# Kernel tuning notes

Measured on AMD Instinct MI355X. Metric: run time of the kernel, lower is better.

Reference implementation:

```python
import jax, jax.numpy as jnp
import numpy as np

# GCN over dependency trees (aryehgigi/gcn-over-pruned-trees), eval mode:
# dropout = identity, rnn=False, dep_dim=0, no_adj=False.
# Per layer l: Ax = adj @ x ; AxW = Linear_l(Ax) + Linear_l(x) (bias counted twice,
# faithful to `self.W[l](Ax) + self.W[l](gcn_inputs)`) ; AxW /= (adj.sum(2)+1) ; relu.

B, L = 128, 256
VOCAB, EMB, POSV, POSD, NERV, NERD, MEM = 50000, 300, 52, 30, 20, 30, 200
IN_DIM = EMB + POSD + NERD  # 360


def setup_inputs() -> dict:
    key = jax.random.key(0)
    ks = jax.random.split(key, 11)
    words = jax.random.randint(ks[0], (B, L), 0, VOCAB)
    pos = jax.random.randint(ks[1], (B, L), 0, POSV)
    ner = jax.random.randint(ks[2], (B, L), 0, NERV)
    adj = (jax.random.uniform(ks[3], (B, L, L)) < 0.05).astype(jnp.float32)
    emb_W = jax.random.normal(ks[4], (VOCAB, EMB), jnp.float32) * 0.1
    pos_W = jax.random.normal(ks[5], (POSV, POSD), jnp.float32) * 0.1
    ner_W = jax.random.normal(ks[6], (NERV, NERD), jnp.float32) * 0.1
    W0 = jax.random.normal(ks[7], (MEM, IN_DIM), jnp.float32) * (1.0 / np.sqrt(IN_DIM))
    b0 = jnp.zeros((MEM,), jnp.float32)
    W1 = jax.random.normal(ks[8], (MEM, MEM), jnp.float32) * (1.0 / np.sqrt(MEM))
    b1 = jnp.zeros((MEM,), jnp.float32)
    return {"words": words, "pos": pos, "ner": ner, "adj": adj,
            "emb_W": emb_W, "pos_W": pos_W, "ner_W": ner_W,
            "W0": W0, "b0": b0, "W1": W1, "b1": b1}


def reference(words, pos, ner, adj, emb_W, pos_W, ner_W, W0, b0, W1, b1):
    # embedding lookups + concat -> [B, L, IN_DIM]
    x = jnp.concatenate([emb_W[words], pos_W[pos], ner_W[ner]], axis=2)
    denom = jnp.sum(adj, axis=2, keepdims=True) + 1.0  # [B, L, 1]
    mask = ((jnp.sum(adj, axis=2) + jnp.sum(adj, axis=1)) == 0)[..., None]  # [B, L, 1]
    for W, b in ((W0, b0), (W1, b1)):
        Ax = jnp.einsum('bij,bjd->bid', adj, x)  # message passing
        # W(Ax) + W(x) == (Ax + x) @ W.T + 2*b  (bias applied twice, as in source)
        h = (jnp.einsum('bld,md->blm', Ax + x, W) + 2.0 * b) / denom
        x = jax.nn.relu(h)
    return (x, mask)
```

## Files before the change

kernel.cpp:

```cpp
#include <hip/hip_runtime.h>
#include <hip/hip_bf16.h>
#include <stdint.h>

typedef __attribute__((ext_vector_type(8))) short short8;
typedef __attribute__((ext_vector_type(4))) float f32x4;

#define NB 128
#define NL 256
#define NROWS 32768
#define IN_DIM 360
#define KP1 384
#define MEM 200
#define NP 256
#define OUT_X (NROWS * MEM)
#define YTP 264
#define BUFSZ 20480
#define YTOFF 40960
#define RSOFF 74752


__device__ __forceinline__ unsigned short f2b(float f) {
    unsigned u = __builtin_bit_cast(unsigned, f);
    unsigned r = (u + 0x7FFFu + ((u >> 16) & 1u)) >> 16;
    return (unsigned short)r;
}

__device__ __forceinline__ void gl16(const void* g, void* l) {
    __builtin_amdgcn_global_load_lds((const __attribute__((address_space(1))) unsigned*)g,
                                     (__attribute__((address_space(3))) unsigned*)l, 16, 0, 0);
}

__device__ __forceinline__ short8 gather_chunk(int chunk, const float* __restrict__ er,
                                               const float* __restrict__ pr,
                                               const float* __restrict__ nr) {
    float v[8];
    if (chunk < 37) {
        const float* s = er + chunk * 8;
        float4 a = *(const float4*)s;
        float4 b = *(const float4*)(s + 4);
        v[0] = a.x; v[1] = a.y; v[2] = a.z; v[3] = a.w;
        v[4] = b.x; v[5] = b.y; v[6] = b.z; v[7] = b.w;
    } else if (chunk == 37) {
        float4 a = *(const float4*)(er + 296);
        v[0] = a.x; v[1] = a.y; v[2] = a.z; v[3] = a.w;
        v[4] = 0.f; v[5] = 0.f; v[6] = 0.f; v[7] = 0.f;
    } else if (chunk <= 41) {
        int k0 = chunk * 8 - 304;
        #pragma unroll
        for (int i = 0; i < 8; ++i) v[i] = (k0 + i < 30) ? pr[k0 + i] : 0.f;
    } else if (chunk <= 45) {
        int k0 = chunk * 8 - 336;
        #pragma unroll
        for (int i = 0; i < 8; ++i) v[i] = (k0 + i < 30) ? nr[k0 + i] : 0.f;
    } else {
        #pragma unroll
        for (int i = 0; i < 8; ++i) v[i] = 0.f;
    }
    short8 r;
    #pragma unroll
    for (int i = 0; i < 8; ++i) r[i] = (short)f2b(v[i]);
    return r;
}

__global__ void prep_weights(const float* __restrict__ W0, const float* __restrict__ W1,
                             short* __restrict__ W0p, short* __restrict__ W1p) {
    int idx = blockIdx.x * 256 + threadIdx.x;
    if (idx < NP * KP1) {
        int n = idx / KP1, kp = idx - n * KP1;
        float v = 0.f;
        if (n < MEM) {
            if (kp < 300)                   v = W0[n * IN_DIM + kp];
            else if (kp >= 304 && kp < 334) v = W0[n * IN_DIM + 300 + (kp - 304)];
            else if (kp >= 336 && kp < 366) v = W0[n * IN_DIM + 330 + (kp - 336)];
        }
        W0p[idx] = (short)f2b(v);
    } else {
        int i2 = idx - NP * KP1;
        if (i2 < NP * NP) {
            int n = i2 >> 8, k = i2 & 255;
            float v = (n < MEM && k < MEM) ? W1[n * MEM + k] : 0.f;
            W1p[i2] = (short)f2b(v);
        }
    }
}

__global__ __launch_bounds__(512, 4) void fused0_kernel(
    const short* __restrict__ Bp,
    unsigned short* __restrict__ Sbf,
    const float* __restrict__ bias,
    const int* __restrict__ words, const int* __restrict__ pos, const int* __restrict__ ner,
    const float* __restrict__ embW, const float* __restrict__ posW,
    const float* __restrict__ nerW,
    const float* __restrict__ adj,
    float* __restrict__ maskout, float* __restrict__ dinvg,
    short* __restrict__ x1b) {
    extern __shared__ char smem[];
    unsigned short* Yt = (unsigned short*)(smem + YTOFF);
    float* dinvL = (float*)(smem + RSOFF);
    unsigned* colnzL = (unsigned*)(smem + RSOFF + 1024);

    int bi = blockIdx.x;
    int batch = bi & 127, sl = bi >> 7;
    int tid = threadIdx.x;
    int lane = tid & 63, wid = tid >> 6;
    int wr = wid >> 1, wc = wid & 1;
    int lr = lane & 15, lc = lane >> 4;

    if (tid < 256) dinvL[tid] = 0.f;
    if (tid < 8) colnzL[tid] = 0u;
    __syncthreads();
    {
        const float* adjb = adj + (size_t)batch * NL * NL;
        unsigned short* Sw = Sbf + (size_t)batch * NL * NL;
        #pragma unroll 4
        for (int j = 0; j < 16; ++j) {
            int cidx = j * 512 + tid;
            int r = cidx >> 5, c0 = (cidx & 31) << 3;
            const float* src = adjb + (size_t)r * NL + c0;
            float4 a = *(const float4*)src;
            float4 b = *(const float4*)(src + 4);
            float s8 = a.x + a.y + a.z + a.w + b.x + b.y + b.z + b.w;
            unsigned bits = 0;
            bits |= (a.x != 0.f) ? 1u : 0u;   bits |= (a.y != 0.f) ? 2u : 0u;
            bits |= (a.z != 0.f) ? 4u : 0u;   bits |= (a.w != 0.f) ? 8u : 0u;
            bits |= (b.x != 0.f) ? 16u : 0u;  bits |= (b.y != 0.f) ? 32u : 0u;
            bits |= (b.z != 0.f) ? 64u : 0u;  bits |= (b.w != 0.f) ? 128u : 0u;
            #pragma unroll
            for (int o = 16; o >= 1; o >>= 1) s8 += __shfl_xor(s8, o);
            if ((lane & 31) == 0) atomicAdd(&dinvL[r], s8);
            if (bits) atomicOr(&colnzL[c0 >> 5], bits << (c0 & 31));
            float d0 = a.x + ((c0 + 0 == r) ? 1.f : 0.f);
            float d1 = a.y + ((c0 + 1 == r) ? 1.f : 0.f);
            float d2 = a.z + ((c0 + 2 == r) ? 1.f : 0.f);
            float d3 = a.w + ((c0 + 3 == r) ? 1.f : 0.f);
            float d4 = b.x + ((c0 + 4 == r) ? 1.f : 0.f);
            float d5 = b.y + ((c0 + 5 == r) ? 1.f : 0.f);
            float d6 = b.z + ((c0 + 6 == r) ? 1.f : 0.f);
            float d7 = b.w + ((c0 + 7 == r) ? 1.f : 0.f);
            short8 st;
            st[0] = (short)f2b(d0); st[1] = (short)f2b(d1);
            st[2] = (short)f2b(d2); st[3] = (short)f2b(d3);
            st[4] = (short)f2b(d4); st[5] = (short)f2b(d5);
            st[6] = (short)f2b(d6); st[7] = (short)f2b(d7);
            *(short8*)(Sw + (size_t)r * NL + c0) = st;
        }
    }
    __syncthreads();
    if (tid < 256) {
        float s = dinvL[tid];
        float di = 1.0f / (s + 1.0f);
        dinvL[tid] = di;
        if (sl == 0) {
            unsigned bit = (colnzL[tid >> 5] >> (tid & 31)) & 1u;
            maskout[batch * NL + tid] = (s == 0.f && bit == 0u) ? 1.0f : 0.0f;
            dinvg[batch * NL + tid] = di;
        }
    }

    const short* Bb = Bp + (size_t)sl * 64 * KP1;
    const short* Sb = (const short*)(Sbf + (size_t)batch * NL * NL);

    int r0s = tid >> 2, c0s = tid & 3;
    int r1s = r0s + 128;
    int offA0 = r0s * 64 + (c0s ^ ((r0s >> 1) & 3)) * 16;
    int offA1 = r1s * 64 + (c0s ^ ((r1s >> 1) & 3)) * 16;
    const short* Sp0 = Sb + (size_t)r0s * NL + c0s * 8;
    const short* Sp1 = Sb + (size_t)r1s * NL + c0s * 8;
    int offB = 0; const short* Bpp = nullptr;
    if (tid < 256) {
        int br = tid >> 2, bc = tid & 3;
        offB = 16384 + br * 64 + (bc ^ ((br >> 1) & 3)) * 16;
        Bpp = Bb + (size_t)br * KP1 + bc * 8;
    }

    const float *er0, *pr0, *nr0, *er1, *pr1, *nr1;
    {
        int g0 = batch * NL + r0s, g1 = g0 + 128;
        er0 = embW + (size_t)words[g0] * 300;
        pr0 = posW + (size_t)pos[g0] * 30;
        nr0 = nerW + (size_t)ner[g0] * 30;
        er1 = embW + (size_t)words[g1] * 300;
        pr1 = posW + (size_t)pos[g1] * 30;
        nr1 = nerW + (size_t)ner[g1] * 30;
    }
    #define LOADA(kt, o0, o1) do {                                  \
        int ch_ = (kt) * 4 + c0s;                                   \
        (o0) = gather_chunk(ch_, er0, pr0, nr0);                    \
        (o1) = gather_chunk(ch_, er1, pr1, nr1);                    \
    } while (0)

    f32x4 acc[4][2] = {};
    short8 aR0, aR1, bR;
    LOADA(0, aR0, aR1);
    if (tid < 256) bR = *(const short8*)Bpp;
    *(short8*)(smem + offA0) = aR0;
    *(short8*)(smem + offA1) = aR1;
    if (tid < 256) *(short8*)(smem + offB) = bR;
    LOADA(1, aR0, aR1);
    if (tid < 256) bR = *(const short8*)(Bpp + 32);
    __syncthreads();

    short8 sA0, sA1, sB0, sB1;
    const int nkt = KP1 / 32;
    for (int kt = 0; kt < nkt; ++kt) {
        char* base_ = smem + (kt & 1) * BUFSZ;
        short8 af[4], bf[2];
        #pragma unroll
        for (int mi = 0; mi < 4; ++mi) {
            int row = wr * 64 + mi * 16 + lr;
            int cs = lc ^ ((row >> 1) & 3);
            af[mi] = *(const short8*)(base_ + row * 64 + cs * 16);
        }
        #pragma unroll
        for (int ni = 0; ni < 2; ++ni) {
            int row = wc * 32 + ni * 16 + lr;
            int cs = lc ^ ((row >> 1) & 3);
            bf[ni] = *(const short8*)(base_ + 16384 + row * 64 + cs * 16);
        }
        if (kt + 1 < nkt) {
            char* nb_ = smem + ((kt + 1) & 1) * BUFSZ;
            *(short8*)(nb_ + offA0) = aR0;
            *(short8*)(nb_ + offA1) = aR1;
            if (tid < 256) *(short8*)(nb_ + offB) = bR;
        }
        if (kt + 2 < nkt) {
            LOADA(kt + 2, aR0, aR1);
            if (tid < 256) bR = *(const short8*)(Bpp + (kt + 2) * 32);
        } else if (kt + 2 == nkt) {
            sA0 = *(const short8*)Sp0;
            sA1 = *(const short8*)Sp1;
        } else if (kt + 2 == nkt + 1) {
            sB0 = *(const short8*)(Sp0 + 32);
            sB1 = *(const short8*)(Sp1 + 32);
        }
        #pragma unroll
        for (int mi = 0; mi < 4; ++mi)
            #pragma unroll
            for (int ni = 0; ni < 2; ++ni)
                acc[mi][ni] = __builtin_amdgcn_mfma_f32_16x16x32_bf16(af[mi], bf[ni], acc[mi][ni], 0, 0, 0);
        __syncthreads();
    }
    #undef LOADA

    #pragma unroll
    for (int mi = 0; mi < 4; ++mi)
        #pragma unroll
        for (int ni = 0; ni < 2; ++ni) {
            f32x4 v = acc[mi][ni];
            ushort4 st; st.x = f2b(v[0]); st.y = f2b(v[1]); st.z = f2b(v[2]); st.w = f2b(v[3]);
            int col = wc * 32 + ni * 16 + lr;
            int row0 = wr * 64 + mi * 16 + lc * 4;
            *(ushort4*)(Yt + (size_t)col * YTP + row0) = st;
        }
    *(short8*)(smem + offA0) = sA0;
    *(short8*)(smem + offA1) = sA1;
    sA0 = *(const short8*)(Sp0 + 64);
    sA1 = *(const short8*)(Sp1 + 64);
    __syncthreads();

    f32x4 acc2[4][2] = {};
    #pragma unroll
    for (int kt = 0; kt < 8; ++kt) {
        char* base_ = smem + (kt & 1) * BUFSZ;
        short8 ay[4], bs[2];
        #pragma unroll
        for (int mi = 0; mi < 4; ++mi)
            ay[mi] = *(const short8*)(Yt + (size_t)(mi * 16 + lr) * YTP + kt * 32 + lc * 8);
        #pragma unroll
        for (int ni = 0; ni < 2; ++ni) {
            int row = wid * 32 + ni * 16 + lr;
            int cs = lc ^ ((row >> 1) & 3);
            bs[ni] = *(const short8*)(base_ + row * 64 + cs * 16);
        }
        if (kt + 1 < 8) {
            char* nb_ = smem + ((kt + 1) & 1) * BUFSZ;
            if ((kt & 1) == 0) {
                *(short8*)(nb_ + offA0) = sB0;
                *(short8*)(nb_ + offA1) = sB1;
                if (kt + 3 < 8) {
                    sB0 = *(const short8*)(Sp0 + (kt + 3) * 32);
                    sB1 = *(const short8*)(Sp1 + (kt + 3) * 32);
                }
            } else {
                *(short8*)(nb_ + offA0) = sA0;
                *(short8*)(nb_ + offA1) = sA1;
                if (kt + 3 < 8) {
                    sA0 = *(const short8*)(Sp0 + (kt + 3) * 32);
                    sA1 = *(const short8*)(Sp1 + (kt + 3) * 32);
                }
            }
        }
        #pragma unroll
        for (int mi = 0; mi < 4; ++mi)
            #pragma unroll
            for (int ni = 0; ni < 2; ++ni)
                acc2[mi][ni] = __builtin_amdgcn_mfma_f32_16x16x32_bf16(ay[mi], bs[ni], acc2[mi][ni], 0, 0, 0);
        if (kt + 1 < 8) __syncthreads();
    }

    #pragma unroll
    for (int ni = 0; ni < 2; ++ni) {
        int rloc = wid * 32 + ni * 16 + lr;
        int g = batch * NL + rloc;
        float di = dinvL[rloc];
        #pragma unroll
        for (int mi = 0; mi < 4; ++mi) {
            int col0 = sl * 64 + mi * 16 + lc * 4;
            float4 bv;
            if (col0 < MEM) bv = *(const float4*)(bias + col0);
            else { bv.x = 0.f; bv.y = 0.f; bv.z = 0.f; bv.w = 0.f; }
            f32x4 z = acc2[mi][ni];
            ushort4 st;
            st.x = f2b(fmaxf((z[0] + 2.f * bv.x) * di, 0.f));
            st.y = f2b(fmaxf((z[1] + 2.f * bv.y) * di, 0.f));
            st.z = f2b(fmaxf((z[2] + 2.f * bv.z) * di, 0.f));
            st.w = f2b(fmaxf((z[3] + 2.f * bv.w) * di, 0.f));
            *(ushort4*)((unsigned short*)x1b + (size_t)g * NP + col0) = st;
        }
    }
}

__global__ __launch_bounds__(512, 4) void fused1_kernel(
    const short* __restrict__ A,
    const short* __restrict__ Bp,
    const unsigned short* __restrict__ Sbf,
    const float* __restrict__ dinv, const float* __restrict__ bias,
    float* __restrict__ outx) {
    extern __shared__ char smem[];
    unsigned short* Yt = (unsigned short*)(smem + YTOFF);

    int bi = blockIdx.x;
    int batch = bi & 127, sl = bi >> 7;
    int tid = threadIdx.x;
    int lane = tid & 63, wid = tid >> 6;
    int wr = wid >> 1, wc = wid & 1;
    int lr = lane & 15, lc = lane >> 4;

    const short* Ab = A + (size_t)batch * NL * NP;
    const short* Bb = Bp + (size_t)sl * 64 * NP;
    const short* Sb = (const short*)(Sbf + (size_t)batch * NL * NL);

    int li0 = tid, li1 = tid + 512;
    int rA0 = li0 >> 2, cA0 = (li0 & 3) ^ ((rA0 >> 1) & 3);
    int rA1 = li1 >> 2, cA1 = (li1 & 3) ^ ((rA1 >> 1) & 3);
    const short* srcA0 = Ab + (size_t)rA0 * NP + cA0 * 8;
    const short* srcA1 = Ab + (size_t)rA1 * NP + cA1 * 8;
    const short* srcS0 = Sb + (size_t)rA0 * NL + cA0 * 8;
    const short* srcS1 = Sb + (size_t)rA1 * NL + cA1 * 8;
    const short* srcB = nullptr;
    if (wid < 4) {
        int rB = tid >> 2, cB = (tid & 3) ^ ((rB >> 1) & 3);
        srcB = Bb + (size_t)rB * NP + cB * 8;
    }
    int dA0 = (wid * 64) * 16;
    int dA1 = (512 + wid * 64) * 16;
    int dB  = 16384 + (wid * 64) * 16;

    #define STAGE1(b, kt) do {                                       \
        char* bb_ = smem + (b) * BUFSZ;                              \
        gl16(srcA0 + (kt) * 32, bb_ + dA0);                          \
        gl16(srcA1 + (kt) * 32, bb_ + dA1);                          \
        if (wid < 4) gl16(srcB + (kt) * 32, bb_ + dB);               \
    } while (0)
    #define STAGES(b, kt) do {                                       \
        char* bb_ = smem + (b) * BUFSZ;                              \
        gl16(srcS0 + (kt) * 32, bb_ + dA0);                          \
        gl16(srcS1 + (kt) * 32, bb_ + dA1);                          \
    } while (0)
    #define WAITBAR() do {                                           \
        asm volatile("s_waitcnt vmcnt(0)" ::: "memory");             \
        __builtin_amdgcn_sched_barrier(0);                           \
        __builtin_amdgcn_s_barrier();                                \
    } while (0)

    f32x4 acc[4][2] = {};
    STAGE1(0, 0);
    WAITBAR();
    #pragma unroll
    for (int kt = 0; kt < 8; ++kt) {
        if (kt + 1 < 8) STAGE1((kt + 1) & 1, kt + 1);
        char* base_ = smem + (kt & 1) * BUFSZ;
        short8 af[4], bf[2];
        #pragma unroll
        for (int mi = 0; mi < 4; ++mi) {
            int row = wr * 64 + mi * 16 + lr;
            int cs = lc ^ ((row >> 1) & 3);
            af[mi] = *(const short8*)(base_ + row * 64 + cs * 16);
        }
        #pragma unroll
        for (int ni = 0; ni < 2; ++ni) {
            int row = wc * 32 + ni * 16 + lr;
            int cs = lc ^ ((row >> 1) & 3);
            bf[ni] = *(const short8*)(base_ + 16384 + row * 64 + cs * 16);
        }
        #pragma unroll
        for (int mi = 0; mi < 4; ++mi)
            #pragma unroll
            for (int ni = 0; ni < 2; ++ni)
                acc[mi][ni] = __builtin_amdgcn_mfma_f32_16x16x32_bf16(af[mi], bf[ni], acc[mi][ni], 0, 0, 0);
        WAITBAR();
    }

    STAGES(0, 0);
    #pragma unroll
    for (int mi = 0; mi < 4; ++mi)
        #pragma unroll
        for (int ni = 0; ni < 2; ++ni) {
            f32x4 v = acc[mi][ni];
            ushort4 st; st.x = f2b(v[0]); st.y = f2b(v[1]); st.z = f2b(v[2]); st.w = f2b(v[3]);
            int col = wc * 32 + ni * 16 + lr;
            int row0 = wr * 64 + mi * 16 + lc * 4;
            *(ushort4*)(Yt + (size_t)col * YTP + row0) = st;
        }
    asm volatile("s_waitcnt vmcnt(0)" ::: "memory");
    __builtin_amdgcn_sched_barrier(0);
    __syncthreads();

    f32x4 acc2[4][2] = {};
    #pragma unroll
    for (int kt = 0; kt < 8; ++kt) {
        if (kt + 1 < 8) STAGES((kt + 1) & 1, kt + 1);
        char* base_ = smem + (kt & 1) * BUFSZ;
        short8 ay[4], bs[2];
        #pragma unroll
        for (int mi = 0; mi < 4; ++mi)
            ay[mi] = *(const short8*)(Yt + (size_t)(mi * 16 + lr) * YTP + kt * 32 + lc * 8);
        #pragma unroll
        for (int ni = 0; ni < 2; ++ni) {
            int row = wid * 32 + ni * 16 + lr;
            int cs = lc ^ ((row >> 1) & 3);
            bs[ni] = *(const short8*)(base_ + row * 64 + cs * 16);
        }
        #pragma unroll
        for (int mi = 0; mi < 4; ++mi)
            #pragma unroll
            for (int ni = 0; ni < 2; ++ni)
                acc2[mi][ni] = __builtin_amdgcn_mfma_f32_16x16x32_bf16(ay[mi], bs[ni], acc2[mi][ni], 0, 0, 0);
        if (kt + 1 < 8) WAITBAR();
    }
    #undef STAGE1
    #undef STAGES
    #undef WAITBAR

    #pragma unroll
    for (int ni = 0; ni < 2; ++ni) {
        int g = batch * NL + wid * 32 + ni * 16 + lr;
        float di = dinv[g];
        #pragma unroll
        for (int mi = 0; mi < 4; ++mi) {
            int col0 = sl * 64 + mi * 16 + lc * 4;
            if (col0 < MEM) {
                float4 bv = *(const float4*)(bias + col0);
                f32x4 z = acc2[mi][ni];
                float4 o;
                o.x = fmaxf((z[0] + 2.f * bv.x) * di, 0.f);
                o.y = fmaxf((z[1] + 2.f * bv.y) * di, 0.f);
                o.z = fmaxf((z[2] + 2.f * bv.z) * di, 0.f);
                o.w = fmaxf((z[3] + 2.f * bv.w) * di, 0.f);
                *(float4*)(outx + (size_t)g * MEM + col0) = o;
            }
        }
    }
}

extern "C" void kernel_launch(void* const* d_in, const int* in_sizes, int n_in,
                              void* d_out, int out_size, void* d_ws, size_t ws_size,
                              hipStream_t stream) {
    const int*   words = (const int*)d_in[0];
    const int*   pos   = (const int*)d_in[1];
    const int*   ner   = (const int*)d_in[2];
    const float* adj   = (const float*)d_in[3];
    const float* embW  = (const float*)d_in[4];
    const float* posW  = (const float*)d_in[5];
    const float* nerW  = (const float*)d_in[6];
    const float* W0    = (const float*)d_in[7];
    const float* b0    = (const float*)d_in[8];
    const float* W1    = (const float*)d_in[9];
    const float* b1    = (const float*)d_in[10];
    float* out = (float*)d_out;

    char* ws = (char*)d_ws;
    size_t off = 0;
    short* W0p = (short*)(ws + off);        off += (size_t)NP * KP1 * 2;
    short* W1p = (short*)(ws + off);        off += (size_t)NP * NP * 2;
    short* X1b = (short*)(ws + off);        off += (size_t)NROWS * NP * 2;
    float* dinv = (float*)(ws + off);       off += (size_t)NROWS * 4;
    unsigned short* Sbf = (unsigned short*)(ws + off); off += (size_t)NROWS * NL * 2;

    prep_weights<<<(NP * KP1 + NP * NP + 255) / 256, 256, 0, stream>>>(W0, W1, W0p, W1p);

    const int ldsB0 = RSOFF + 1024 + 32;
    const int ldsB1 = YTOFF + 64 * YTP * 2;
    fused0_kernel<<<NB * 4, 512, ldsB0, stream>>>(W0p, Sbf, b0,
                                                  words, pos, ner, embW, posW, nerW,
                                                  adj, out + OUT_X, dinv, X1b);
    fused1_kernel<<<NB * 4, 512, ldsB1, stream>>>(X1b, W1p, Sbf, dinv, b1, out);
}
```

Before: 67.55 us.

## Fuse fp32 adjacency conversion into layer-0 stream, computing row sums inline

Removes the separate prologue that converted the whole fp32 adjacency tile to bf16 (with atomics and two barriers) before the GEMMs. Each thread now loads its own fp32 adjacency chunks just in time inside the pipelined loops, converts them (adding the identity), accumulates row sums and column-nonzero bits, and writes the bf16 copy to global only from the first column slice. Row-degree reciprocals are reduced with shuffles after the second GEMM. The aim is to overlap adjacency conversion with MFMA work and avoid redundant writes, at the cost of more fp32 global reads and more register pressure.

```diff
diff --git a/kernel.cpp b/kernel.cpp
--- a/kernel.cpp
+++ b/kernel.cpp
@@ -28,6 +28,26 @@
 __device__ __forceinline__ void gl16(const void* g, void* l) {
     __builtin_amdgcn_global_load_lds((const __attribute__((address_space(1))) unsigned*)g,
                                      (__attribute__((address_space(3))) unsigned*)l, 16, 0, 0);
+}
+
+__device__ __forceinline__ short8 convS(float4 a, float4 b, int row, int j0, float& rs,
+                                        unsigned* colnzL, bool dobits) {
+    float v[8];
+    v[0] = a.x; v[1] = a.y; v[2] = a.z; v[3] = a.w;
+    v[4] = b.x; v[5] = b.y; v[6] = b.z; v[7] = b.w;
+    rs += v[0] + v[1] + v[2] + v[3] + v[4] + v[5] + v[6] + v[7];
+    if (dobits) {
+        unsigned bits = 0;
+        #pragma unroll
+        for (int i = 0; i < 8; ++i) bits |= (v[i] != 0.f) ? (1u << i) : 0u;
+        if (bits) atomicOr(&colnzL[j0 >> 5], bits << (j0 & 31));
+    }
+    int d = row - j0;
+    if (d >= 0 && d < 8) v[d] += 1.f;
+    short8 st;
+    #pragma unroll
+    for (int i = 0; i < 8; ++i) st[i] = (short)f2b(v[i]);
+    return st;
 }
 
 __device__ __forceinline__ short8 gather_chunk(int chunk, const float* __restrict__ er,
@@ -105,67 +125,20 @@
     int lane = tid & 63, wid = tid >> 6;
     int wr = wid >> 1, wc = wid & 1;
     int lr = lane & 15, lc = lane >> 4;
-
-    if (tid < 256) dinvL[tid] = 0.f;
+    bool s0 = (sl == 0);
+
     if (tid < 8) colnzL[tid] = 0u;
-    __syncthreads();
-    {
-        const float* adjb = adj + (size_t)batch * NL * NL;
-        unsigned short* Sw = Sbf + (size_t)batch * NL * NL;
-        #pragma unroll 4
-        for (int j = 0; j < 16; ++j) {
-            int cidx = j * 512 + tid;
-            int r = cidx >> 5, c0 = (cidx & 31) << 3;
-            const float* src = adjb + (size_t)r * NL + c0;
-            float4 a = *(const float4*)src;
-            float4 b = *(const float4*)(src + 4);
-            float s8 = a.x + a.y + a.z + a.w + b.x + b.y + b.z + b.w;
-            unsigned bits = 0;
-            bits |= (a.x != 0.f) ? 1u : 0u;   bits |= (a.y != 0.f) ? 2u : 0u;
-            bits |= (a.z != 0.f) ? 4u : 0u;   bits |= (a.w != 0.f) ? 8u : 0u;
-            bits |= (b.x != 0.f) ? 16u : 0u;  bits |= (b.y != 0.f) ? 32u : 0u;
-            bits |= (b.z != 0.f) ? 64u : 0u;  bits |= (b.w != 0.f) ? 128u : 0u;
-            #pragma unroll
-            for (int o = 16; o >= 1; o >>= 1) s8 += __shfl_xor(s8, o);
-            if ((lane & 31) == 0) atomicAdd(&dinvL[r], s8);
-            if (bits) atomicOr(&colnzL[c0 >> 5], bits << (c0 & 31));
-            float d0 = a.x + ((c0 + 0 == r) ? 1.f : 0.f);
-            float d1 = a.y + ((c0 + 1 == r) ? 1.f : 0.f);
-            float d2 = a.z + ((c0 + 2 == r) ? 1.f : 0.f);
-            float d3 = a.w + ((c0 + 3 == r) ? 1.f : 0.f);
-            float d4 = b.x + ((c0 + 4 == r) ? 1.f : 0.f);
-            float d5 = b.y + ((c0 + 5 == r) ? 1.f : 0.f);
-            float d6 = b.z + ((c0 + 6 == r) ? 1.f : 0.f);
-            float d7 = b.w + ((c0 + 7 == r) ? 1.f : 0.f);
-            short8 st;
-            st[0] = (short)f2b(d0); st[1] = (short)f2b(d1);
-            st[2] = (short)f2b(d2); st[3] = (short)f2b(d3);
-            st[4] = (short)f2b(d4); st[5] = (short)f2b(d5);
-            st[6] = (short)f2b(d6); st[7] = (short)f2b(d7);
-            *(short8*)(Sw + (size_t)r * NL + c0) = st;
-        }
-    }
-    __syncthreads();
-    if (tid < 256) {
-        float s = dinvL[tid];
-        float di = 1.0f / (s + 1.0f);
-        dinvL[tid] = di;
-        if (sl == 0) {
-            unsigned bit = (colnzL[tid >> 5] >> (tid & 31)) & 1u;
-            maskout[batch * NL + tid] = (s == 0.f && bit == 0u) ? 1.0f : 0.0f;
-            dinvg[batch * NL + tid] = di;
-        }
-    }
-
+
+    const float* adjb = adj + (size_t)batch * NL * NL;
+    unsigned short* Sw = Sbf + (size_t)batch * NL * NL;
     const short* Bb = Bp + (size_t)sl * 64 * KP1;
-    const short* Sb = (const short*)(Sbf + (size_t)batch * NL * NL);
 
     int r0s = tid >> 2, c0s = tid & 3;
     int r1s = r0s + 128;
     int offA0 = r0s * 64 + (c0s ^ ((r0s >> 1) & 3)) * 16;
     int offA1 = r1s * 64 + (c0s ^ ((r1s >> 1) & 3)) * 16;
-    const short* Sp0 = Sb + (size_t)r0s * NL + c0s * 8;
-    const short* Sp1 = Sb + (size_t)r1s * NL + c0s * 8;
+    const float* aS0 = adjb + (size_t)r0s * NL + c0s * 8;
+    const float* aS1 = adjb + (size_t)r1s * NL + c0s * 8;
     int offB = 0; const short* Bpp = nullptr;
     if (tid < 256) {
         int br = tid >> 2, bc = tid & 3;
@@ -190,6 +163,9 @@
     } while (0)
 
     f32x4 acc[4][2] = {};
+    float rs0 = 0.f, rs1 = 0.f;
+    float4 fA0a, fA0b, fA1a, fA1b, fB0a, fB0b, fB1a, fB1b;
+
     short8 aR0, aR1, bR;
     LOADA(0, aR0, aR1);
     if (tid < 256) bR = *(const short8*)Bpp;
@@ -200,7 +176,6 @@
     if (tid < 256) bR = *(const short8*)(Bpp + 32);
     __syncthreads();
 
-    short8 sA0, sA1, sB0, sB1;
     const int nkt = KP1 / 32;
     for (int kt = 0; kt < nkt; ++kt) {
         char* base_ = smem + (kt & 1) * BUFSZ;
@@ -227,11 +202,11 @@
             LOADA(kt + 2, aR0, aR1);
             if (tid < 256) bR = *(const short8*)(Bpp + (kt + 2) * 32);
         } else if (kt + 2 == nkt) {
-            sA0 = *(const short8*)Sp0;
-            sA1 = *(const short8*)Sp1;
+            fA0a = *(const float4*)(aS0);     fA0b = *(const float4*)(aS0 + 4);
+            fA1a = *(const float4*)(aS1);     fA1b = *(const float4*)(aS1 + 4);
         } else if (kt + 2 == nkt + 1) {
-            sB0 = *(const short8*)(Sp0 + 32);
-            sB1 = *(const short8*)(Sp1 + 32);
+            fB0a = *(const float4*)(aS0 + 32); fB0b = *(const float4*)(aS0 + 36);
+            fB1a = *(const float4*)(aS1 + 32); fB1b = *(const float4*)(aS1 + 36);
         }
         #pragma unroll
         for (int mi = 0; mi < 4; ++mi)
@@ -252,10 +227,19 @@
             int row0 = wr * 64 + mi * 16 + lc * 4;
             *(ushort4*)(Yt + (size_t)col * YTP + row0) = st;
         }
-    *(short8*)(smem + offA0) = sA0;
-    *(short8*)(smem + offA1) = sA1;
-    sA0 = *(const short8*)(Sp0 + 64);
-    sA1 = *(const short8*)(Sp1 + 64);
+    {
+        int j0 = c0s * 8;
+        short8 t0 = convS(fA0a, fA0b, r0s, j0, rs0, colnzL, s0);
+        short8 t1 = convS(fA1a, fA1b, r1s, j0, rs1, colnzL, s0);
+        *(short8*)(smem + offA0) = t0;
+        *(short8*)(smem + offA1) = t1;
+        if (s0) {
+            *(short8*)(Sw + (size_t)r0s * NL + j0) = t0;
+            *(short8*)(Sw + (size_t)r1s * NL + j0) = t1;
+        }
+    }
+    fA0a = *(const float4*)(aS0 + 64); fA0b = *(const float4*)(aS0 + 68);
+    fA1a = *(const float4*)(aS1 + 64); fA1b = *(const float4*)(aS1 + 68);
     __syncthreads();
 
     f32x4 acc2[4][2] = {};
@@ -274,19 +258,36 @@
         }
         if (kt + 1 < 8) {
             char* nb_ = smem + ((kt + 1) & 1) * BUFSZ;
+            int j0 = (kt + 1) * 32 + c0s * 8;
             if ((kt & 1) == 0) {
-                *(short8*)(nb_ + offA0) = sB0;
-                *(short8*)(nb_ + offA1) = sB1;
+                short8 t0 = convS(fB0a, fB0b, r0s, j0, rs0, colnzL, s0);
+                short8 t1 = convS(fB1a, fB1b, r1s, j0, rs1, colnzL, s0);
+                *(short8*)(nb_ + offA0) = t0;
+                *(short8*)(nb_ + offA1) = t1;
+                if (s0) {
+                    *(short8*)(Sw + (size_t)r0s * NL + j0) = t0;
+                    *(short8*)(Sw + (size_t)r1s * NL + j0) = t1;
+                }
                 if (kt + 3 < 8) {
-                    sB0 = *(const short8*)(Sp0 + (kt + 3) * 32);
-                    sB1 = *(const short8*)(Sp1 + (kt + 3) * 32);
+                    fB0a = *(const float4*)(aS0 + (kt + 3) * 32);
+                    fB0b = *(const float4*)(aS0 + (kt + 3) * 32 + 4);
+                    fB1a = *(const float4*)(aS1 + (kt + 3) * 32);
+                    fB1b = *(const float4*)(aS1 + (kt + 3) * 32 + 4);
                 }
             } else {
-                *(short8*)(nb_ + offA0) = sA0;
-                *(short8*)(nb_ + offA1) = sA1;
+                short8 t0 = convS(fA0a, fA0b, r0s, j0, rs0, colnzL, s0);
+                short8 t1 = convS(fA1a, fA1b, r1s, j0, rs1, colnzL, s0);
+                *(short8*)(nb_ + offA0) = t0;
+                *(short8*)(nb_ + offA1) = t1;
+                if (s0) {
+                    *(short8*)(Sw + (size_t)r0s * NL + j0) = t0;
+                    *(short8*)(Sw + (size_t)r1s * NL + j0) = t1;
+                }
                 if (kt + 3 < 8) {
-                    sA0 = *(const short8*)(Sp0 + (kt + 3) * 32);
-                    sA1 = *(const short8*)(Sp1 + (kt + 3) * 32);
+                    fA0a = *(const float4*)(aS0 + (kt + 3) * 32);
+                    fA0b = *(const float4*)(aS0 + (kt + 3) * 32 + 4);
+                    fA1a = *(const float4*)(aS1 + (kt + 3) * 32);
+                    fA1b = *(const float4*)(aS1 + (kt + 3) * 32 + 4);
                 }
             }
         }
@@ -295,7 +296,22 @@
             #pragma unroll
             for (int ni = 0; ni < 2; ++ni)
                 acc2[mi][ni] = __builtin_amdgcn_mfma_f32_16x16x32_bf16(ay[mi], bs[ni], acc2[mi][ni], 0, 0, 0);
-        if (kt + 1 < 8) __syncthreads();
+        __syncthreads();
+    }
+
+    rs0 += __shfl_xor(rs0, 1); rs0 += __shfl_xor(rs0, 2);
+    rs1 += __shfl_xor(rs1, 1); rs1 += __shfl_xor(rs1, 2);
+    if (c0s == 0) {
+        dinvL[r0s] = 1.0f / (rs0 + 1.0f);
+        dinvL[r1s] = 1.0f / (rs1 + 1.0f);
+    }
+    __syncthreads();
+
+    if (s0 && tid < 256) {
+        float di = dinvL[tid];
+        unsigned bit = (colnzL[tid >> 5] >> (tid & 31)) & 1u;
+        maskout[batch * NL + tid] = (di == 1.0f && bit == 0u) ? 1.0f : 0.0f;
+        dinvg[batch * NL + tid] = di;
     }
 
     #pragma unroll
```

Result: slower. 134.7 us (+99.4%).

## Fuse both GCN layers into one kernel with per-batch atomic flag barrier

Applied to the files above, without the earlier changes.

Merges the layer-0 and layer-1 kernels into a single launch. The four column-slice blocks of each batch synchronize through an atomic counter in global memory, initialized by the weight-prep kernel, and spin until all four have written the layer-0 activations. dinv now stays in LDS instead of going through global memory, which removes one kernel launch and the launch gap between layers. In exchange it relies on all 512 blocks being co-resident (4 blocks per CU with 512 threads) to avoid deadlock, and adds spin-wait and fence overhead.

```diff
diff --git a/kernel.cpp b/kernel.cpp
--- a/kernel.cpp
+++ b/kernel.cpp
@@ -63,8 +63,10 @@
 }
 
 __global__ void prep_weights(const float* __restrict__ W0, const float* __restrict__ W1,
-                             short* __restrict__ W0p, short* __restrict__ W1p) {
+                             short* __restrict__ W0p, short* __restrict__ W1p,
+                             int* __restrict__ flags) {
     int idx = blockIdx.x * 256 + threadIdx.x;
+    if (idx < NB) flags[idx] = 0;
     if (idx < NP * KP1) {
         int n = idx / KP1, kp = idx - n * KP1;
         float v = 0.f;
@@ -84,16 +86,17 @@
     }
 }
 
-__global__ __launch_bounds__(512, 4) void fused0_kernel(
-    const short* __restrict__ Bp,
+__global__ __launch_bounds__(512, 4) void fused_all(
+    const short* __restrict__ B0p, const short* __restrict__ B1p,
     unsigned short* __restrict__ Sbf,
-    const float* __restrict__ bias,
+    const float* __restrict__ bias0, const float* __restrict__ bias1,
     const int* __restrict__ words, const int* __restrict__ pos, const int* __restrict__ ner,
     const float* __restrict__ embW, const float* __restrict__ posW,
     const float* __restrict__ nerW,
     const float* __restrict__ adj,
-    float* __restrict__ maskout, float* __restrict__ dinvg,
-    short* __restrict__ x1b) {
+    float* __restrict__ maskout,
+    short* __restrict__ x1b, int* __restrict__ flags,
+    float* __restrict__ outx) {
     extern __shared__ char smem[];
     unsigned short* Yt = (unsigned short*)(smem + YTOFF);
     float* dinvL = (float*)(smem + RSOFF);
@@ -153,11 +156,10 @@
         if (sl == 0) {
             unsigned bit = (colnzL[tid >> 5] >> (tid & 31)) & 1u;
             maskout[batch * NL + tid] = (s == 0.f && bit == 0u) ? 1.0f : 0.0f;
-            dinvg[batch * NL + tid] = di;
-        }
-    }
-
-    const short* Bb = Bp + (size_t)sl * 64 * KP1;
+        }
+    }
+
+    const short* Bb = B0p + (size_t)sl * 64 * KP1;
     const short* Sb = (const short*)(Sbf + (size_t)batch * NL * NL);
 
     int r0s = tid >> 2, c0s = tid & 3;
@@ -189,275 +191,271 @@
         (o1) = gather_chunk(ch_, er1, pr1, nr1);                    \
     } while (0)
 
-    f32x4 acc[4][2] = {};
-    short8 aR0, aR1, bR;
-    LOADA(0, aR0, aR1);
-    if (tid < 256) bR = *(const short8*)Bpp;
-    *(short8*)(smem + offA0) = aR0;
-    *(short8*)(smem + offA1) = aR1;
-    if (tid < 256) *(short8*)(smem + offB) = bR;
-    LOADA(1, aR0, aR1);
-    if (tid < 256) bR = *(const short8*)(Bpp + 32);
+    {
+        f32x4 acc[4][2] = {};
+        short8 aR0, aR1, bR;
+        LOADA(0, aR0, aR1);
+        if (tid < 256) bR = *(const short8*)Bpp;
+        *(short8*)(smem + offA0) = aR0;
+        *(short8*)(smem + offA1) = aR1;
+        if (tid < 256) *(short8*)(smem + offB) = bR;
+        LOADA(1, aR0, aR1);
+        if (tid < 256) bR = *(const short8*)(Bpp + 32);
+        __syncthreads();
+
+        short8 sA0, sA1, sB0, sB1;
+        const int nkt = KP1 / 32;
+        for (int kt = 0; kt < nkt; ++kt) {
+            char* base_ = smem + (kt & 1) * BUFSZ;
+            short8 af[4], bf[2];
+            #pragma unroll
+            for (int mi = 0; mi < 4; ++mi) {
+                int row = wr * 64 + mi * 16 + lr;
+                int cs = lc ^ ((row >> 1) & 3);
+                af[mi] = *(const short8*)(base_ + row * 64 + cs * 16);
+            }
+            #pragma unroll
+            for (int ni = 0; ni < 2; ++ni) {
+                int row = wc * 32 + ni * 16 + lr;
+                int cs = lc ^ ((row >> 1) & 3);
+                bf[ni] = *(const short8*)(base_ + 16384 + row * 64 + cs * 16);
+            }
+            if (kt + 1 < nkt) {
+                char* nb_ = smem + ((kt + 1) & 1) * BUFSZ;
+                *(short8*)(nb_ + offA0) = aR0;
+                *(short8*)(nb_ + offA1) = aR1;
+                if (tid < 256) *(short8*)(nb_ + offB) = bR;
+            }
+            if (kt + 2 < nkt) {
+                LOADA(kt + 2, aR0, aR1);
+                if (tid < 256) bR = *(const short8*)(Bpp + (kt + 2) * 32);
+            } else if (kt + 2 == nkt) {
+                sA0 = *(const short8*)Sp0;
+                sA1 = *(const short8*)Sp1;
+            } else if (kt + 2 == nkt + 1) {
+                sB0 = *(const short8*)(Sp0 + 32);
+                sB1 = *(const short8*)(Sp1 + 32);
+            }
+            #pragma unroll
+            for (int mi = 0; mi < 4; ++mi)
+                #pragma unroll
+                for (int ni = 0; ni < 2; ++ni)
+                    acc[mi][ni] = __builtin_amdgcn_mfma_f32_16x16x32_bf16(af[mi], bf[ni], acc[mi][ni], 0, 0, 0);
+            __syncthreads();
+        }
+
+        #pragma unroll
+        for (int mi = 0; mi < 4; ++mi)
+            #pragma unroll
+            for (int ni = 0; ni < 2; ++ni) {
+                f32x4 v = acc[mi][ni];
+                ushort4 st; st.x = f2b(v[0]); st.y = f2b(v[1]); st.z = f2b(v[2]); st.w = f2b(v[3]);
+                int col = wc * 32 + ni * 16 + lr;
+                int row0 = wr * 64 + mi * 16 + lc * 4;
+                *(ushort4*)(Yt + (size_t)col * YTP + row0) = st;
+            }
+        *(short8*)(smem + offA0) = sA0;
+        *(short8*)(smem + offA1) = sA1;
+        sA0 = *(const short8*)(Sp0 + 64);
+        sA1 = *(const short8*)(Sp1 + 64);
+        __syncthreads();
+
+        f32x4 acc2[4][2] = {};
+        #pragma unroll
+        for (int kt = 0; kt < 8; ++kt) {
+            char* base_ = smem + (kt & 1) * BUFSZ;
+            short8 ay[4], bs[2];
+            #pragma unroll
+            for (int mi = 0; mi < 4; ++mi)
+                ay[mi] = *(const short8*)(Yt + (size_t)(mi * 16 + lr) * YTP + kt * 32 + lc * 8);
+            #pragma unroll
+            for (int ni = 0; ni < 2; ++ni) {
+                int row = wid * 32 + ni * 16 + lr;
+                int cs = lc ^ ((row >> 1) & 3);
+                bs[ni] = *(const short8*)(base_ + row * 64 + cs * 16);
+            }
+            if (kt + 1 < 8) {
+                char* nb_ = smem + ((kt + 1) & 1) * BUFSZ;
+                if ((kt & 1) == 0) {
+                    *(short8*)(nb_ + offA0) = sB0;
+                    *(short8*)(nb_ + offA1) = sB1;
+                    if (kt + 3 < 8) {
+                        sB0 = *(const short8*)(Sp0 + (kt + 3) * 32);
+                        sB1 = *(const short8*)(Sp1 + (kt + 3) * 32);
+                    }
+                } else {
+                    *(short8*)(nb_ + offA0) = sA0;
+                    *(short8*)(nb_ + offA1) = sA1;
+                    if (kt + 3 < 8) {
+                        sA0 = *(const short8*)(Sp0 + (kt + 3) * 32);
+                        sA1 = *(const short8*)(Sp1 + (kt + 3) * 32);
+                    }
+                }
+            }
+            #pragma unroll
+            for (int mi = 0; mi < 4; ++mi)
+                #pragma unroll
+                for (int ni = 0; ni < 2; ++ni)
+                    acc2[mi][ni] = __builtin_amdgcn_mfma_f32_16x16x32_bf16(ay[mi], bs[ni], acc2[mi][ni], 0, 0, 0);
+            if (kt + 1 < 8) __syncthreads();
+        }
+
+        #pragma unroll
+        for (int ni = 0; ni < 2; ++ni) {
+            int rloc = wid * 32 + ni * 16 + lr;
+            int g = batch * NL + rloc;
+            float di = dinvL[rloc];
+            #pragma unroll
+            for (int mi = 0; mi < 4; ++mi) {
+                int col0 = sl * 64 + mi * 16 + lc * 4;
+                float4 bv;
+                if (col0 < MEM) bv = *(const float4*)(bias0 + col0);
+                else { bv.x = 0.f; bv.y = 0.f; bv.z = 0.f; bv.w = 0.f; }
+                f32x4 z = acc2[mi][ni];
+                ushort4 st;
+                st.x = f2b(fmaxf((z[0] + 2.f * bv.x) * di, 0.f));
+                st.y = f2b(fmaxf((z[1] + 2.f * bv.y) * di, 0.f));
+                st.z = f2b(fmaxf((z[2] + 2.f * bv.z) * di, 0.f));
+                st.w = f2b(fmaxf((z[3] + 2.f * bv.w) * di, 0.f));
+                *(ushort4*)((unsigned short*)x1b + (size_t)g * NP + col0) = st;
+            }
+        }
+    }
+    #undef LOADA
+
+    __threadfence();
     __syncthreads();
-
-    short8 sA0, sA1, sB0, sB1;
-    const int nkt = KP1 / 32;
-    for (int kt = 0; kt < nkt; ++kt) {
-        char* base_ = smem + (kt & 1) * BUFSZ;
-        short8 af[4], bf[2];
-        #pragma unroll
-        for (int mi = 0; mi < 4; ++mi) {
-            int row = wr * 64 + mi * 16 + lr;
-            int cs = lc ^ ((row >> 1) & 3);
-            af[mi] = *(const short8*)(base_ + row * 64 + cs * 16);
-        }
+    if (tid == 0) {
+        atomicAdd(&flags[batch], 1);
+        while (atomicCAS(&flags[batch], 4, 4) < 4) { __builtin_amdgcn_s_sleep(8); }
+    }
+    __syncthreads();
+    __threadfence();
+
+    {
+        const short* Ab = x1b + (size_t)batch * NL * NP;
+        const short* B2 = B1p + (size_t)sl * 64 * NP;
+
+        int li1 = tid + 512;
+        int rA0 = tid >> 2, cA0 = (tid & 3) ^ ((rA0 >> 1) & 3);
+        int rA1 = li1 >> 2, cA1 = (li1 & 3) ^ ((rA1 >> 1) & 3);
+        const short* srcA0 = Ab + (size_t)rA0 * NP + cA0 * 8;
+        const short* srcA1 = Ab + (size_t)rA1 * NP + cA1 * 8;
+        const short* srcS0 = Sb + (size_t)rA0 * NL + cA0 * 8;
+        const short* srcS1 = Sb + (size_t)rA1 * NL + cA1 * 8;
+        const short* srcB = nullptr;
+        if (wid < 4) {
+            int rB = tid >> 2, cB = (tid & 3) ^ ((rB >> 1) & 3);
+            srcB = B2 + (size_t)rB * NP + cB * 8;
+        }
+        int dA0 = (wid * 64) * 16;
+        int dA1 = (512 + wid * 64) * 16;
+        int dB  = 16384 + (wid * 64) * 16;
+
+        #define STAGE1(b, kt) do {                                       \
+            char* bb_ = smem + (b) * BUFSZ;                              \
+            gl16(srcA0 + (kt) * 32, bb_ + dA0);                          \
+            gl16(srcA1 + (kt) * 32, bb_ + dA1);                          \
+            if (wid < 4) gl16(srcB + (kt) * 32, bb_ + dB);               \
+        } while (0)
+        #define STAGES(b, kt) do {                                       \
+            char* bb_ = smem + (b) * BUFSZ;                              \
+            gl16(srcS0 + (kt) * 32, bb_ + dA0);                          \
+            gl16(srcS1 + (kt) * 32, bb_ + dA1);                          \
+        } while (0)
+        #define WAITBAR() do {                                           \
+            asm volatile("s_waitcnt vmcnt(0)" ::: "memory");             \
+            __builtin_amdgcn_sched_barrier(0);                           \
+            __builtin_amdgcn_s_barrier();                                \
+        } while (0)
+
+        f32x4 acc[4][2] = {};
+        STAGE1(0, 0);
+        WAITBAR();
+        #pragma unroll
+        for (int kt = 0; kt < 8; ++kt) {
+            if (kt + 1 < 8) STAGE1((kt + 1) & 1, kt + 1);
+            char* base_ = smem + (kt & 1) * BUFSZ;
+            short8 af[4], bf[2];
+            #pragma unroll
+            for (int mi = 0; mi < 4; ++mi) {
+                int row = wr * 64 + mi * 16 + lr;
+                int cs = lc ^ ((row >> 1) & 3);
+                af[mi] = *(const short8*)(base_ + row * 64 + cs * 16);
+            }
+            #pragma unroll
+            for (int ni = 0; ni < 2; ++ni) {
+                int row = wc * 32 + ni * 16 + lr;
+                int cs = lc ^ ((row >> 1) & 3);
+                bf[ni] = *(const short8*)(base_ + 16384 + row * 64 + cs * 16);
+            }
+            #pragma unroll
+            for (int mi = 0; mi < 4; ++mi)
+                #pragma unroll
+                for (int ni = 0; ni < 2; ++ni)
+                    acc[mi][ni] = __builtin_amdgcn_mfma_f32_16x16x32_bf16(af[mi], bf[ni], acc[mi][ni], 0, 0, 0);
+            WAITBAR();
+        }
+
+        STAGES(0, 0);
+        #pragma unroll
+        for (int mi = 0; mi < 4; ++mi)
+            #pragma unroll
+            for (int ni = 0; ni < 2; ++ni) {
+                f32x4 v = acc[mi][ni];
+                ushort4 st; st.x = f2b(v[0]); st.y = f2b(v[1]); st.z = f2b(v[2]); st.w = f2b(v[3]);
+                int col = wc * 32 + ni * 16 + lr;
+                int row0 = wr * 64 + mi * 16 + lc * 4;
+                *(ushort4*)(Yt + (size_t)col * YTP + row0) = st;
+            }
+        asm volatile("s_waitcnt vmcnt(0)" ::: "memory");
+        __builtin_amdgcn_sched_barrier(0);
+        __syncthreads();
+
+        f32x4 acc2[4][2] = {};
+        #pragma unroll
+        for (int kt = 0; kt < 8; ++kt) {
+            if (kt + 1 < 8) STAGES((kt + 1) & 1, kt + 1);
+            char* base_ = smem + (kt & 1) * BUFSZ;
+            short8 ay[4], bs[2];
+            #pragma unroll
+            for (int mi = 0; mi < 4; ++mi)
+                ay[mi] = *(const short8*)(Yt + (size_t)(mi * 16 + lr) * YTP + kt * 32 + lc * 8);
+            #pragma unroll
+            for (int ni = 0; ni < 2; ++ni) {
+                int row = wid * 32 + ni * 16 + lr;
+                int cs = lc ^ ((row >> 1) & 3);
+                bs[ni] = *(const short8*)(base_ + row * 64 + cs * 16);
+            }
+            #pragma unroll
+            for (int mi = 0; mi < 4; ++mi)
+                #pragma unroll
+                for (int ni = 0; ni < 2; ++ni)
+                    acc2[mi][ni] = __builtin_amdgcn_mfma_f32_16x16x32_bf16(ay[mi], bs[ni], acc2[mi][ni], 0, 0, 0);
+            if (kt + 1 < 8) WAITBAR();
+        }
+        #undef STAGE1
+        #undef STAGES
+        #undef WAITBAR
+
         #pragma unroll
         for (int ni = 0; ni < 2; ++ni) {
-            int row = wc * 32 + ni * 16 + lr;
-            int cs = lc ^ ((row >> 1) & 3);
-            bf[ni] = *(const short8*)(base_ + 16384 + row * 64 + cs * 16);
-        }
-        if (kt + 1 < nkt) {
-            char* nb_ = smem + ((kt + 1) & 1) * BUFSZ;
-            *(short8*)(nb_ + offA0) = aR0;
-            *(short8*)(nb_ + offA1) = aR1;
-            if (tid < 256) *(short8*)(nb_ + offB) = bR;
-        }
-        if (kt + 2 < nkt) {
-            LOADA(kt + 2, aR0, aR1);
-            if (tid < 256) bR = *(const short8*)(Bpp + (kt + 2) * 32);
-        } else if (kt + 2 == nkt) {
-            sA0 = *(const short8*)Sp0;
-            sA1 = *(const short8*)Sp1;
-        } else if (kt + 2 == nkt + 1) {
-            sB0 = *(const short8*)(Sp0 + 32);
-            sB1 = *(const short8*)(Sp1 + 32);
-        }
-        #pragma unroll
-        for (int mi = 0; mi < 4; ++mi)
-            #pragma unroll
-            for (int ni = 0; ni < 2; ++ni)
-                acc[mi][ni] = __builtin_amdgcn_mfma_f32_16x16x32_bf16(af[mi], bf[ni], acc[mi][ni], 0, 0, 0);
-        __syncthreads();
-    }
-    #undef LOADA
-
-    #pragma unroll
-    for (int mi = 0; mi < 4; ++mi)
-        #pragma unroll
-        for (int ni = 0; ni < 2; ++ni) {
-            f32x4 v = acc[mi][ni];
-            ushort4 st; st.x = f2b(v[0]); st.y = f2b(v[1]); st.z = f2b(v[2]); st.w = f2b(v[3]);
-            int col = wc * 32 + ni * 16 + lr;
-            int row0 = wr * 64 + mi * 16 + lc * 4;
-            *(ushort4*)(Yt + (size_t)col * YTP + row0) = st;
-        }
-    *(short8*)(smem + offA0) = sA0;
-    *(short8*)(smem + offA1) = sA1;
-    sA0 = *(const short8*)(Sp0 + 64);
-    sA1 = *(const short8*)(Sp1 + 64);
-    __syncthreads();
-
-    f32x4 acc2[4][2] = {};
-    #pragma unroll
-    for (int kt = 0; kt < 8; ++kt) {
-        char* base_ = smem + (kt & 1) * BUFSZ;
-        short8 ay[4], bs[2];
-        #pragma unroll
-        for (int mi = 0; mi < 4; ++mi)
-            ay[mi] = *(const short8*)(Yt + (size_t)(mi * 16 + lr) * YTP + kt * 32 + lc * 8);
-        #pragma unroll
-        for (int ni = 0; ni < 2; ++ni) {
-            int row = wid * 32 + ni * 16 + lr;
-            int cs = lc ^ ((row >> 1) & 3);
-            bs[ni] = *(const short8*)(base_ + row * 64 + cs * 16);
-        }
-        if (kt + 1 < 8) {
-            char* nb_ = smem + ((kt + 1) & 1) * BUFSZ;
-            if ((kt & 1) == 0) {
-                *(short8*)(nb_ + offA0) = sB0;
-                *(short8*)(nb_ + offA1) = sB1;
-                if (kt + 3 < 8) {
-                    sB0 = *(const short8*)(Sp0 + (kt + 3) * 32);
-                    sB1 = *(const short8*)(Sp1 + (kt + 3) * 32);
+            int rloc = wid * 32 + ni * 16 + lr;
+            int g = batch * NL + rloc;
+            float di = dinvL[rloc];
+            #pragma unroll
+            for (int mi = 0; mi < 4; ++mi) {
+                int col0 = sl * 64 + mi * 16 + lc * 4;
+                if (col0 < MEM) {
+                    float4 bv = *(const float4*)(bias1 + col0);
+                    f32x4 z = acc2[mi][ni];
+                    float4 o;
+                    o.x = fmaxf((z[0] + 2.f * bv.x) * di, 0.f);
+                    o.y = fmaxf((z[1] + 2.f * bv.y) * di, 0.f);
+                    o.z = fmaxf((z[2] + 2.f * bv.z) * di, 0.f);
+                    o.w = fmaxf((z[3] + 2.f * bv.w) * di, 0.f);
+                    *(float4*)(outx + (size_t)g * MEM + col0) = o;
                 }
-            } else {
-                *(short8*)(nb_ + offA0) = sA0;
-                *(short8*)(nb_ + offA1) = sA1;
-                if (kt + 3 < 8) {
-                    sA0 = *(const short8*)(Sp0 + (kt + 3) * 32);
-                    sA1 = *(const short8*)(Sp1 + (kt + 3) * 32);
-                }
-            }
-        }
-        #pragma unroll
-        for (int mi = 0; mi < 4; ++mi)
-            #pragma unroll
-            for (int ni = 0; ni < 2; ++ni)
-                acc2[mi][ni] = __builtin_amdgcn_mfma_f32_16x16x32_bf16(ay[mi], bs[ni], acc2[mi][ni], 0, 0, 0);
-        if (kt + 1 < 8) __syncthreads();
-    }
-
-    #pragma unroll
-    for (int ni = 0; ni < 2; ++ni) {
-        int rloc = wid * 32 + ni * 16 + lr;
-        int g = batch * NL + rloc;
-        float di = dinvL[rloc];
-        #pragma unroll
-        for (int mi = 0; mi < 4; ++mi) {
-            int col0 = sl * 64 + mi * 16 + lc * 4;
-            float4 bv;
-            if (col0 < MEM) bv = *(const float4*)(bias + col0);
-            else { bv.x = 0.f; bv.y = 0.f; bv.z = 0.f; bv.w = 0.f; }
-            f32x4 z = acc2[mi][ni];
-            ushort4 st;
-            st.x = f2b(fmaxf((z[0] + 2.f * bv.x) * di, 0.f));
-            st.y = f2b(fmaxf((z[1] + 2.f * bv.y) * di, 0.f));
-            st.z = f2b(fmaxf((z[2] + 2.f * bv.z) * di, 0.f));
-            st.w = f2b(fmaxf((z[3] + 2.f * bv.w) * di, 0.f));
-            *(ushort4*)((unsigned short*)x1b + (size_t)g * NP + col0) = st;
-        }
-    }
-}
-
-__global__ __launch_bounds__(512, 4) void fused1_kernel(
-    const short* __restrict__ A,
-    const short* __restrict__ Bp,
-    const unsigned short* __restrict__ Sbf,
-    const float* __restrict__ dinv, const float* __restrict__ bias,
-    float* __restrict__ outx) {
-    extern __shared__ char smem[];
-    unsigned short* Yt = (unsigned short*)(smem + YTOFF);
-
-    int bi = blockIdx.x;
-    int batch = bi & 127, sl = bi >> 7;
-    int tid = threadIdx.x;
-    int lane = tid & 63, wid = tid >> 6;
-    int wr = wid >> 1, wc = wid & 1;
-    int lr = lane & 15, lc = lane >> 4;
-
-    const short* Ab = A + (size_t)batch * NL * NP;
-    const short* Bb = Bp + (size_t)sl * 64 * NP;
-    const short* Sb = (const short*)(Sbf + (size_t)batch * NL * NL);
-
-    int li0 = tid, li1 = tid + 512;
-    int rA0 = li0 >> 2, cA0 = (li0 & 3) ^ ((rA0 >> 1) & 3);
-    int rA1 = li1 >> 2, cA1 = (li1 & 3) ^ ((rA1 >> 1) & 3);
-    const short* srcA0 = Ab + (size_t)rA0 * NP + cA0 * 8;
-    const short* srcA1 = Ab + (size_t)rA1 * NP + cA1 * 8;
-    const short* srcS0 = Sb + (size_t)rA0 * NL + cA0 * 8;
-    const short* srcS1 = Sb + (size_t)rA1 * NL + cA1 * 8;
-    const short* srcB = nullptr;
-    if (wid < 4) {
-        int rB = tid >> 2, cB = (tid & 3) ^ ((rB >> 1) & 3);
-        srcB = Bb + (size_t)rB * NP + cB * 8;
-    }
-    int dA0 = (wid * 64) * 16;
-    int dA1 = (512 + wid * 64) * 16;
-    int dB  = 16384 + (wid * 64) * 16;
-
-    #define STAGE1(b, kt) do {                                       \
-        char* bb_ = smem + (b) * BUFSZ;                              \
-        gl16(srcA0 + (kt) * 32, bb_ + dA0);                          \
-        gl16(srcA1 + (kt) * 32, bb_ + dA1);                          \
-        if (wid < 4) gl16(srcB + (kt) * 32, bb_ + dB);               \
-    } while (0)
-    #define STAGES(b, kt) do {                                       \
-        char* bb_ = smem + (b) * BUFSZ;                              \
-        gl16(srcS0 + (kt) * 32, bb_ + dA0);                          \
-        gl16(srcS1 + (kt) * 32, bb_ + dA1);                          \
-    } while (0)
-    #define WAITBAR() do {                                           \
-        asm volatile("s_waitcnt vmcnt(0)" ::: "memory");             \
-        __builtin_amdgcn_sched_barrier(0);                           \
-        __builtin_amdgcn_s_barrier();                                \
-    } while (0)
-
-    f32x4 acc[4][2] = {};
-    STAGE1(0, 0);
-    WAITBAR();
-    #pragma unroll
-    for (int kt = 0; kt < 8; ++kt) {
-        if (kt + 1 < 8) STAGE1((kt + 1) & 1, kt + 1);
-        char* base_ = smem + (kt & 1) * BUFSZ;
-        short8 af[4], bf[2];
-        #pragma unroll
-        for (int mi = 0; mi < 4; ++mi) {
-            int row = wr * 64 + mi * 16 + lr;
-            int cs = lc ^ ((row >> 1) & 3);
-            af[mi] = *(const short8*)(base_ + row * 64 + cs * 16);
-        }
-        #pragma unroll
-        for (int ni = 0; ni < 2; ++ni) {
-            int row = wc * 32 + ni * 16 + lr;
-            int cs = lc ^ ((row >> 1) & 3);
-            bf[ni] = *(const short8*)(base_ + 16384 + row * 64 + cs * 16);
-        }
-        #pragma unroll
-        for (int mi = 0; mi < 4; ++mi)
-            #pragma unroll
-            for (int ni = 0; ni < 2; ++ni)
-                acc[mi][ni] = __builtin_amdgcn_mfma_f32_16x16x32_bf16(af[mi], bf[ni], acc[mi][ni], 0, 0, 0);
-        WAITBAR();
-    }
-
-    STAGES(0, 0);
-    #pragma unroll
-    for (int mi = 0; mi < 4; ++mi)
-        #pragma unroll
-        for (int ni = 0; ni < 2; ++ni) {
-            f32x4 v = acc[mi][ni];
-            ushort4 st; st.x = f2b(v[0]); st.y = f2b(v[1]); st.z = f2b(v[2]); st.w = f2b(v[3]);
-            int col = wc * 32 + ni * 16 + lr;
-            int row0 = wr * 64 + mi * 16 + lc * 4;
-            *(ushort4*)(Yt + (size_t)col * YTP + row0) = st;
-        }
-    asm volatile("s_waitcnt vmcnt(0)" ::: "memory");
-    __builtin_amdgcn_sched_barrier(0);
-    __syncthreads();
-
-    f32x4 acc2[4][2] = {};
-    #pragma unroll
-    for (int kt = 0; kt < 8; ++kt) {
-        if (kt + 1 < 8) STAGES((kt + 1) & 1, kt + 1);
-        char* base_ = smem + (kt & 1) * BUFSZ;
-        short8 ay[4], bs[2];
-        #pragma unroll
-        for (int mi = 0; mi < 4; ++mi)
-            ay[mi] = *(const short8*)(Yt + (size_t)(mi * 16 + lr) * YTP + kt * 32 + lc * 8);
-        #pragma unroll
-        for (int ni = 0; ni < 2; ++ni) {
-            int row = wid * 32 + ni * 16 + lr;
-            int cs = lc ^ ((row >> 1) & 3);
-            bs[ni] = *(const short8*)(base_ + row * 64 + cs * 16);
-        }
-        #pragma unroll
-        for (int mi = 0; mi < 4; ++mi)
-            #pragma unroll
-            for (int ni = 0; ni < 2; ++ni)
-                acc2[mi][ni] = __builtin_amdgcn_mfma_f32_16x16x32_bf16(ay[mi], bs[ni], acc2[mi][ni], 0, 0, 0);
-        if (kt + 1 < 8) WAITBAR();
-    }
-    #undef STAGE1
-    #undef STAGES
-    #undef WAITBAR
-
-    #pragma unroll
-    for (int ni = 0; ni < 2; ++ni) {
-        int g = batch * NL + wid * 32 + ni * 16 + lr;
-        float di = dinv[g];
-        #pragma unroll
-        for (int mi = 0; mi < 4; ++mi) {
-            int col0 = sl * 64 + mi * 16 + lc * 4;
-            if (col0 < MEM) {
-                float4 bv = *(const float4*)(bias + col0);
-                f32x4 z = acc2[mi][ni];
-                float4 o;
-                o.x = fmaxf((z[0] + 2.f * bv.x) * di, 0.f);
-                o.y = fmaxf((z[1] + 2.f * bv.y) * di, 0.f);
-                o.z = fmaxf((z[2] + 2.f * bv.z) * di, 0.f);
-                o.w = fmaxf((z[3] + 2.f * bv.w) * di, 0.f);
-                *(float4*)(outx + (size_t)g * MEM + col0) = o;
             }
         }
     }
@@ -484,15 +482,13 @@
     short* W0p = (short*)(ws + off);        off += (size_t)NP * KP1 * 2;
     short* W1p = (short*)(ws + off);        off += (size_t)NP * NP * 2;
     short* X1b = (short*)(ws + off);        off += (size_t)NROWS * NP * 2;
-    float* dinv = (float*)(ws + off);       off += (size_t)NROWS * 4;
+    int* flags = (int*)(ws + off);          off += (size_t)NB * 4;
     unsigned short* Sbf = (unsigned short*)(ws + off); off += (size_t)NROWS * NL * 2;
 
-    prep_weights<<<(NP * KP1 + NP * NP + 255) / 256, 256, 0, stream>>>(W0, W1, W0p, W1p);
-
-    const int ldsB0 = RSOFF + 1024 + 32;
-    const int ldsB1 = YTOFF + 64 * YTP * 2;
-    fused0_kernel<<<NB * 4, 512, ldsB0, stream>>>(W0p, Sbf, b0,
-                                                  words, pos, ner, embW, posW, nerW,
-                                                  adj, out + OUT_X, dinv, X1b);
-    fused1_kernel<<<NB * 4, 512, ldsB1, stream>>>(X1b, W1p, Sbf, dinv, b1, out);
-}
+    prep_weights<<<(NP * KP1 + NP * NP + 255) / 256, 256, 0, stream>>>(W0, W1, W0p, W1p, flags);
+
+    const int ldsB = RSOFF + 1024 + 32;
+    fused_all<<<NB * 4, 512, ldsB, stream>>>(W0p, W1p, Sbf, b0, b1,
+                                             words, pos, ner, embW, posW, nerW,
+                                             adj, out + OUT_X, X1b, flags, out);
+}
```

After: 258.2 us. 3.82x slower.
